# Kernel optimization log

Measured on AMD Instinct MI355X. Metric: run time of the kernel, lower is better.

Reference implementation:

```python
import jax, jax.numpy as jnp
import numpy as np

H = 4  # heads


def _tconv(x, src, dst, ea, Wq, bq, Wk, bk, Wv, bv, We, Ws, bs):
    # PyG TransformerConv, heads=4, concat=False, root_weight=True, beta=False
    N = x.shape[0]
    Dh = Wq.shape[1] // H  # per-head dim (= hidden_channels)
    q = (x @ Wq + bq).reshape(N, H, Dh)
    k = (x @ Wk + bk).reshape(N, H, Dh)
    v = (x @ Wv + bv).reshape(N, H, Dh)
    e = (ea @ We).reshape(-1, H, Dh)      # lin_edge has no bias in PyG
    kj = k[src] + e                        # [E, H, Dh]
    vj = v[src] + e                        # [E, H, Dh]
    alpha = (q[dst] * kj).sum(-1) / jnp.sqrt(jnp.asarray(Dh, x.dtype))  # [E, H]
    # segment softmax over incoming edges of each dst node
    m = jax.ops.segment_max(alpha, dst, num_segments=N)
    a = jnp.exp(alpha - m[dst])
    s = jax.ops.segment_sum(a, dst, num_segments=N)
    a = a / (s[dst] + 1e-16)
    out = jax.ops.segment_sum(a[:, :, None] * vj, dst, num_segments=N)  # [N, H, Dh]
    out = out.mean(axis=1)                 # concat=False -> mean over heads
    return out + x @ Ws + bs               # root/skip connection


def setup_inputs() -> dict:
    key = jax.random.key(0)
    ks = jax.random.split(key, 32)
    N, E, C_in, C_e, Ch = 50000, 800000, 32, 16, 32
    d = {}
    d['x'] = jax.random.normal(ks[0], (N, C_in), dtype=jnp.float32)
    d['edge_attr'] = jax.random.normal(ks[1], (E, C_e), dtype=jnp.float32)
    d['edge_index'] = jax.random.randint(ks[2], (2, E), 0, N, dtype=jnp.int32)
    s = 0.05
    i = 3
    for L, cin in ((1, C_in), (2, Ch)):
        d[f'Wq{L}'] = jax.random.normal(ks[i], (cin, H * Ch)) * s; i += 1
        d[f'bq{L}'] = jnp.zeros((H * Ch,), jnp.float32)
        d[f'Wk{L}'] = jax.random.normal(ks[i], (cin, H * Ch)) * s; i += 1
        d[f'bk{L}'] = jnp.zeros((H * Ch,), jnp.float32)
        d[f'Wv{L}'] = jax.random.normal(ks[i], (cin, H * Ch)) * s; i += 1
        d[f'bv{L}'] = jnp.zeros((H * Ch,), jnp.float32)
        d[f'We{L}'] = jax.random.normal(ks[i], (C_e, H * Ch)) * s; i += 1
        d[f'Ws{L}'] = jax.random.normal(ks[i], (cin, Ch)) * s; i += 1
        d[f'bs{L}'] = jnp.zeros((Ch,), jnp.float32)
    d['Wm1'] = jax.random.normal(ks[i], (2 * Ch + C_e, Ch)) * s; i += 1
    d['bm1'] = jnp.zeros((Ch,), jnp.float32)
    d['Wm2'] = jax.random.normal(ks[i], (Ch, 1)) * s; i += 1
    d['bm2'] = jnp.zeros((1,), jnp.float32)
    return d


def reference(x, edge_attr, edge_index,
              Wq1, bq1, Wk1, bk1, Wv1, bv1, We1, Ws1, bs1,
              Wq2, bq2, Wk2, bk2, Wv2, bv2, We2, Ws2, bs2,
              Wm1, bm1, Wm2, bm2):
    src, dst = edge_index[0], edge_index[1]
    h = jax.nn.relu(_tconv(x, src, dst, edge_attr, Wq1, bq1, Wk1, bk1, Wv1, bv1, We1, Ws1, bs1))
    h = jax.nn.relu(_tconv(h, src, dst, edge_attr, Wq2, bq2, Wk2, bk2, Wv2, bv2, We2, Ws2, bs2))
    ef = jnp.concatenate([h[src], edge_attr, h[dst]], axis=-1)  # [E, 2*Ch + C_e]
    out = jax.nn.relu(ef @ Wm1 + bm1) @ Wm2 + bm2
    return out.reshape(-1)
```

## Files before the change

kernel.cpp:

```cpp
#include <hip/hip_runtime.h>
#include <math.h>

#define D128 128
#define CH32 32
#define CE16 16

__global__ void k_hist(const int* __restrict__ dst, int* __restrict__ deg, int E) {
    int e = blockIdx.x * blockDim.x + threadIdx.x;
    if (e < E) atomicAdd(&deg[dst[e]], 1);
}

__global__ void k_scan1(const int* __restrict__ deg, int* __restrict__ offs,
                        int* __restrict__ bsum, int N) {
    __shared__ int buf[256];
    int t = threadIdx.x;
    int i = blockIdx.x * 256 + t;
    int v = (i < N) ? deg[i] : 0;
    buf[t] = v;
    __syncthreads();
    #pragma unroll
    for (int off = 1; off < 256; off <<= 1) {
        int val = (t >= off) ? buf[t - off] : 0;
        __syncthreads();
        buf[t] += val;
        __syncthreads();
    }
    if (i < N) offs[i] = buf[t] - v;
    if (t == 255) bsum[blockIdx.x] = buf[255];
}

__global__ void k_scan2(const int* __restrict__ bsum, int* __restrict__ boff, int nb) {
    __shared__ int buf[256];
    int t = threadIdx.x;
    int v = (t < nb) ? bsum[t] : 0;
    buf[t] = v;
    __syncthreads();
    #pragma unroll
    for (int off = 1; off < 256; off <<= 1) {
        int val = (t >= off) ? buf[t - off] : 0;
        __syncthreads();
        buf[t] += val;
        __syncthreads();
    }
    if (t < nb) boff[t] = buf[t] - v;
}

__global__ void k_scan3(const int* __restrict__ boff, int* __restrict__ offs,
                        int* __restrict__ cur, int N, int E) {
    int i = blockIdx.x * blockDim.x + threadIdx.x;
    if (i < N) {
        int o = offs[i] + boff[i >> 8];
        offs[i] = o;
        cur[i] = o;
    }
    if (i == 0) offs[N] = E;
}

__global__ void k_scatter(const int* __restrict__ src, const int* __restrict__ dst,
                          int* __restrict__ cur, int* __restrict__ csr_srcb,
                          float4* __restrict__ ea_csr4, const float4* __restrict__ ea4,
                          int E) {
    int e = blockIdx.x * blockDim.x + threadIdx.x;
    if (e < E) {
        int d = dst[e];
        int p = atomicAdd(&cur[d], 1);
        csr_srcb[p] = src[e] << 10;
        float4 a0 = ea4[e * 4 + 0];
        float4 a1 = ea4[e * 4 + 1];
        float4 a2 = ea4[e * 4 + 2];
        float4 a3 = ea4[e * 4 + 3];
        ea_csr4[p * 4 + 0] = a0;
        ea_csr4[p * 4 + 1] = a1;
        ea_csr4[p * 4 + 2] = a2;
        ea_csr4[p * 4 + 3] = a3;
    }
}

__global__ __launch_bounds__(128) void k_nodeproj(
    const float* __restrict__ xin,
    const float* __restrict__ Wq, const float* __restrict__ bq,
    const float* __restrict__ Wk, const float* __restrict__ bk,
    const float* __restrict__ Wv, const float* __restrict__ bv,
    const float* __restrict__ Ws, const float* __restrict__ bs,
    float* __restrict__ q, float* __restrict__ kv,
    float* __restrict__ skip, int N)
{
    int tid = threadIdx.x;
    int c   = tid & 31;
    float wq[32], wk[32], wv[32], ws[32];
    #pragma unroll
    for (int j = 0; j < 32; j++) {
        wq[j] = Wq[j * D128 + tid];
        wk[j] = Wk[j * D128 + tid];
        wv[j] = Wv[j * D128 + tid];
        ws[j] = Ws[j * CH32 + c];
    }
    float bqc = bq[tid], bkc = bk[tid], bvc = bv[tid], bsc = bs[c];
    __shared__ float xs[4][32];
    int nchunk = (N + 3) / 4;
    for (int chk = blockIdx.x; chk < nchunk; chk += gridDim.x) {
        int base = chk * 4;
        {
            int r = tid >> 5;
            int n = base + r;
            xs[r][c] = (n < N) ? xin[n * 32 + c] : 0.f;
        }
        __syncthreads();
        #pragma unroll
        for (int r = 0; r < 4; r++) {
            int n = base + r;
            if (n < N) {
                float aq = bqc, ak = bkc, av = bvc;
                #pragma unroll
                for (int j = 0; j < 32; j++) {
                    float xj = xs[r][j];
                    aq = fmaf(xj, wq[j], aq);
                    ak = fmaf(xj, wk[j], ak);
                    av = fmaf(xj, wv[j], av);
                }
                q[n * D128 + tid] = aq;
                kv[(size_t)n * 256 + tid]       = ak;
                kv[(size_t)n * 256 + 128 + tid] = av;
            }
        }
        {
            int r = tid >> 5;
            int n = base + r;
            if (n < N) {
                float as = bsc;
                #pragma unroll
                for (int j = 0; j < 32; j++) as = fmaf(xs[r][j], ws[j], as);
                skip[n * 32 + c] = as;
            }
        }
        __syncthreads();
    }
}

__global__ __launch_bounds__(64) void k_edgeattn(
    const float* __restrict__ q, const float* __restrict__ kv,
    const float* __restrict__ skip,
    const float* __restrict__ ea_csr, const float* __restrict__ We,
    const int* __restrict__ offs, const int* __restrict__ csr_srcb,
    float* __restrict__ hout)
{
    int node = blockIdx.x;
    int lane = threadIdx.x;
    int col2 = lane << 1;

    float2 we[16];
    #pragma unroll
    for (int j = 0; j < 16; j++)
        we[j] = *(const float2*)&We[j * D128 + col2];

    const float QS = 0.17677669529663687f * 1.4426950408889634f;
    float2 qv = *(const float2*)&q[(size_t)node * D128 + col2];
    qv.x *= QS; qv.y *= QS;

    int s0 = offs[node], s1 = offs[node + 1];

    float l = 0.f;
    float ac0 = 0.f, ac1 = 0.f;
    const char* kvb = (const char*)kv;
    int toff = lane * 8;

    int i = s0;
    if ((s1 - s0) & 1) {
        int sa = csr_srcb[i];
        const char* pa = kvb + (size_t)(unsigned)sa + toff;
        float2 ka = *(const float2*)(pa);
        float2 va = *(const float2*)(pa + 512);
        const float4* ea4 = (const float4*)&ea_csr[(size_t)i * 16];
        float4 a0 = ea4[0], a1 = ea4[1], a2 = ea4[2], a3 = ea4[3];

        float e0 = 0.f, e1 = 0.f;
        e0 = fmaf(a0.x, we[0].x,  e0);  e1 = fmaf(a0.x, we[0].y,  e1);
        e0 = fmaf(a0.y, we[1].x,  e0);  e1 = fmaf(a0.y, we[1].y,  e1);
        e0 = fmaf(a0.z, we[2].x,  e0);  e1 = fmaf(a0.z, we[2].y,  e1);
        e0 = fmaf(a0.w, we[3].x,  e0);  e1 = fmaf(a0.w, we[3].y,  e1);
        e0 = fmaf(a1.x, we[4].x,  e0);  e1 = fmaf(a1.x, we[4].y,  e1);
        e0 = fmaf(a1.y, we[5].x,  e0);  e1 = fmaf(a1.y, we[5].y,  e1);
        e0 = fmaf(a1.z, we[6].x,  e0);  e1 = fmaf(a1.z, we[6].y,  e1);
        e0 = fmaf(a1.w, we[7].x,  e0);  e1 = fmaf(a1.w, we[7].y,  e1);
        e0 = fmaf(a2.x, we[8].x,  e0);  e1 = fmaf(a2.x, we[8].y,  e1);
        e0 = fmaf(a2.y, we[9].x,  e0);  e1 = fmaf(a2.y, we[9].y,  e1);
        e0 = fmaf(a2.z, we[10].x, e0);  e1 = fmaf(a2.z, we[10].y, e1);
        e0 = fmaf(a2.w, we[11].x, e0);  e1 = fmaf(a2.w, we[11].y, e1);
        e0 = fmaf(a3.x, we[12].x, e0);  e1 = fmaf(a3.x, we[12].y, e1);
        e0 = fmaf(a3.y, we[13].x, e0);  e1 = fmaf(a3.y, we[13].y, e1);
        e0 = fmaf(a3.z, we[14].x, e0);  e1 = fmaf(a3.z, we[14].y, e1);
        e0 = fmaf(a3.w, we[15].x, e0);  e1 = fmaf(a3.w, we[15].y, e1);

        float kj0 = ka.x + e0, kj1 = ka.y + e1;
        float vj0 = va.x + e0, vj1 = va.y + e1;
        float t = qv.x * kj0;
        t = fmaf(qv.y, kj1, t);
        t += __shfl_xor(t, 1);
        t += __shfl_xor(t, 2);
        t += __shfl_xor(t, 4);
        t += __shfl_xor(t, 8);
        float p = __builtin_amdgcn_exp2f(t);
        l += p;
        ac0 = fmaf(p, vj0, ac0);
        ac1 = fmaf(p, vj1, ac1);
        i++;
    }

    for (; i < s1; i += 2) {
        int sa = csr_srcb[i];
        int sb = csr_srcb[i + 1];
        const char* pa = kvb + (size_t)(unsigned)sa + toff;
        const char* pb = kvb + (size_t)(unsigned)sb + toff;
        float2 ka = *(const float2*)(pa);
        float2 va = *(const float2*)(pa + 512);
        float2 kb = *(const float2*)(pb);
        float2 vb = *(const float2*)(pb + 512);
        const float4* ea4 = (const float4*)&ea_csr[(size_t)i * 16];
        float4 a0 = ea4[0], a1 = ea4[1], a2 = ea4[2], a3 = ea4[3];
        float4 b0 = ea4[4], b1 = ea4[5], b2 = ea4[6], b3 = ea4[7];

        float ea0 = 0.f, ea1 = 0.f, eb0 = 0.f, eb1 = 0.f;
        ea0 = fmaf(a0.x, we[0].x,  ea0);  ea1 = fmaf(a0.x, we[0].y,  ea1);
        eb0 = fmaf(b0.x, we[0].x,  eb0);  eb1 = fmaf(b0.x, we[0].y,  eb1);
        ea0 = fmaf(a0.y, we[1].x,  ea0);  ea1 = fmaf(a0.y, we[1].y,  ea1);
        eb0 = fmaf(b0.y, we[1].x,  eb0);  eb1 = fmaf(b0.y, we[1].y,  eb1);
        ea0 = fmaf(a0.z, we[2].x,  ea0);  ea1 = fmaf(a0.z, we[2].y,  ea1);
        eb0 = fmaf(b0.z, we[2].x,  eb0);  eb1 = fmaf(b0.z, we[2].y,  eb1);
        ea0 = fmaf(a0.w, we[3].x,  ea0);  ea1 = fmaf(a0.w, we[3].y,  ea1);
        eb0 = fmaf(b0.w, we[3].x,  eb0);  eb1 = fmaf(b0.w, we[3].y,  eb1);
        ea0 = fmaf(a1.x, we[4].x,  ea0);  ea1 = fmaf(a1.x, we[4].y,  ea1);
        eb0 = fmaf(b1.x, we[4].x,  eb0);  eb1 = fmaf(b1.x, we[4].y,  eb1);
        ea0 = fmaf(a1.y, we[5].x,  ea0);  ea1 = fmaf(a1.y, we[5].y,  ea1);
        eb0 = fmaf(b1.y, we[5].x,  eb0);  eb1 = fmaf(b1.y, we[5].y,  eb1);
        ea0 = fmaf(a1.z, we[6].x,  ea0);  ea1 = fmaf(a1.z, we[6].y,  ea1);
        eb0 = fmaf(b1.z, we[6].x,  eb0);  eb1 = fmaf(b1.z, we[6].y,  eb1);
        ea0 = fmaf(a1.w, we[7].x,  ea0);  ea1 = fmaf(a1.w, we[7].y,  ea1);
        eb0 = fmaf(b1.w, we[7].x,  eb0);  eb1 = fmaf(b1.w, we[7].y,  eb1);
        ea0 = fmaf(a2.x, we[8].x,  ea0);  ea1 = fmaf(a2.x, we[8].y,  ea1);
        eb0 = fmaf(b2.x, we[8].x,  eb0);  eb1 = fmaf(b2.x, we[8].y,  eb1);
        ea0 = fmaf(a2.y, we[9].x,  ea0);  ea1 = fmaf(a2.y, we[9].y,  ea1);
        eb0 = fmaf(b2.y, we[9].x,  eb0);  eb1 = fmaf(b2.y, we[9].y,  eb1);
        ea0 = fmaf(a2.z, we[10].x, ea0);  ea1 = fmaf(a2.z, we[10].y, ea1);
        eb0 = fmaf(b2.z, we[10].x, eb0);  eb1 = fmaf(b2.z, we[10].y, eb1);
        ea0 = fmaf(a2.w, we[11].x, ea0);  ea1 = fmaf(a2.w, we[11].y, ea1);
        eb0 = fmaf(b2.w, we[11].x, eb0);  eb1 = fmaf(b2.w, we[11].y, eb1);
        ea0 = fmaf(a3.x, we[12].x, ea0);  ea1 = fmaf(a3.x, we[12].y, ea1);
        eb0 = fmaf(b3.x, we[12].x, eb0);  eb1 = fmaf(b3.x, we[12].y, eb1);
        ea0 = fmaf(a3.y, we[13].x, ea0);  ea1 = fmaf(a3.y, we[13].y, ea1);
        eb0 = fmaf(b3.y, we[13].x, eb0);  eb1 = fmaf(b3.y, we[13].y, eb1);
        ea0 = fmaf(a3.z, we[14].x, ea0);  ea1 = fmaf(a3.z, we[14].y, ea1);
        eb0 = fmaf(b3.z, we[14].x, eb0);  eb1 = fmaf(b3.z, we[14].y, eb1);
        ea0 = fmaf(a3.w, we[15].x, ea0);  ea1 = fmaf(a3.w, we[15].y, ea1);
        eb0 = fmaf(b3.w, we[15].x, eb0);  eb1 = fmaf(b3.w, we[15].y, eb1);

        float kja0 = ka.x + ea0, kja1 = ka.y + ea1;
        float vja0 = va.x + ea0, vja1 = va.y + ea1;
        float kjb0 = kb.x + eb0, kjb1 = kb.y + eb1;
        float vjb0 = vb.x + eb0, vjb1 = vb.y + eb1;

        float ta = qv.x * kja0;
        float tb = qv.x * kjb0;
        ta = fmaf(qv.y, kja1, ta);
        tb = fmaf(qv.y, kjb1, tb);

        ta += __shfl_xor(ta, 1);   tb += __shfl_xor(tb, 1);
        ta += __shfl_xor(ta, 2);   tb += __shfl_xor(tb, 2);
        ta += __shfl_xor(ta, 4);   tb += __shfl_xor(tb, 4);
        ta += __shfl_xor(ta, 8);   tb += __shfl_xor(tb, 8);

        float p0 = __builtin_amdgcn_exp2f(ta);
        float p1 = __builtin_amdgcn_exp2f(tb);
        l += p0 + p1;
        ac0 = fmaf(p0, vja0, ac0);
        ac1 = fmaf(p0, vja1, ac1);
        ac0 = fmaf(p1, vjb0, ac0);
        ac1 = fmaf(p1, vjb1, ac1);
    }

    float inv = 1.0f / (l + 1e-16f);
    float r0 = ac0 * inv;
    float r1 = ac1 * inv;
    r0 += __shfl_xor(r0, 16);   r1 += __shfl_xor(r1, 16);
    r0 += __shfl_xor(r0, 32);   r1 += __shfl_xor(r1, 32);
    if (lane < 16) {
        const float2 sk = *(const float2*)&skip[(size_t)node * 32 + col2];
        float o0 = fmaxf(fmaf(0.25f, r0, sk.x), 0.f);
        float o1 = fmaxf(fmaf(0.25f, r1, sk.y), 0.f);
        *(float2*)&hout[(size_t)node * 32 + col2] = make_float2(o0, o1);
    }
}

__global__ __launch_bounds__(256) void k_mlp(
    const float* __restrict__ h, const float* __restrict__ ea,
    const int* __restrict__ src, const int* __restrict__ dst,
    const float* __restrict__ Wm1, const float* __restrict__ bm1,
    const float* __restrict__ Wm2, const float* __restrict__ bm2,
    float* __restrict__ out, int E)
{
    __shared__ float4 W4[80 * 8];
    __shared__ float bm1L[32];
    __shared__ float wm2L[32];
    int tid = threadIdx.x;
    const float4* Wm1_4 = (const float4*)Wm1;
    for (int i = tid; i < 640; i += 256) W4[i] = Wm1_4[i];
    if (tid < 32) { bm1L[tid] = bm1[tid]; wm2L[tid] = Wm2[tid]; }
    __syncthreads();

    int e = blockIdx.x * 256 + tid;
    if (e >= E) return;
    float b2 = bm2[0];
    int s = src[e], d = dst[e];

    float4 acc[8];
    #pragma unroll
    for (int i = 0; i < 8; i++) acc[i] = make_float4(0.f, 0.f, 0.f, 0.f);

    auto dorow = [&](int j, float xj) {
        #pragma unroll
        for (int c4 = 0; c4 < 8; c4++) {
            float4 w = W4[j * 8 + c4];
            acc[c4].x = fmaf(xj, w.x, acc[c4].x);
            acc[c4].y = fmaf(xj, w.y, acc[c4].y);
            acc[c4].z = fmaf(xj, w.z, acc[c4].z);
            acc[c4].w = fmaf(xj, w.w, acc[c4].w);
        }
    };

    const float4* hs  = (const float4*)(h + (size_t)s * 32);
    const float4* hd  = (const float4*)(h + (size_t)d * 32);
    const float4* eav = (const float4*)(ea + (size_t)e * 16);
    #pragma unroll
    for (int qd = 0; qd < 8; qd++) {
        float4 xv = hs[qd];
        dorow(qd * 4 + 0, xv.x); dorow(qd * 4 + 1, xv.y);
        dorow(qd * 4 + 2, xv.z); dorow(qd * 4 + 3, xv.w);
    }
    #pragma unroll
    for (int qd = 0; qd < 4; qd++) {
        float4 xv = eav[qd];
        dorow(32 + qd * 4 + 0, xv.x); dorow(32 + qd * 4 + 1, xv.y);
        dorow(32 + qd * 4 + 2, xv.z); dorow(32 + qd * 4 + 3, xv.w);
    }
    #pragma unroll
    for (int qd = 0; qd < 8; qd++) {
        float4 xv = hd[qd];
        dorow(48 + qd * 4 + 0, xv.x); dorow(48 + qd * 4 + 1, xv.y);
        dorow(48 + qd * 4 + 2, xv.z); dorow(48 + qd * 4 + 3, xv.w);
    }

    float y = b2;
    #pragma unroll
    for (int c4 = 0; c4 < 8; c4++) {
        y += fmaxf(acc[c4].x + bm1L[c4 * 4 + 0], 0.f) * wm2L[c4 * 4 + 0];
        y += fmaxf(acc[c4].y + bm1L[c4 * 4 + 1], 0.f) * wm2L[c4 * 4 + 1];
        y += fmaxf(acc[c4].z + bm1L[c4 * 4 + 2], 0.f) * wm2L[c4 * 4 + 2];
        y += fmaxf(acc[c4].w + bm1L[c4 * 4 + 3], 0.f) * wm2L[c4 * 4 + 3];
    }
    out[e] = y;
}

extern "C" void kernel_launch(void* const* d_in, const int* in_sizes, int n_in,
                              void* d_out, int out_size, void* d_ws, size_t ws_size,
                              hipStream_t stream)
{
    const float* x  = (const float*)d_in[0];
    const float* ea = (const float*)d_in[1];
    const int*   ei = (const int*)d_in[2];
    const int N = in_sizes[0] / 32;
    const int E = in_sizes[1] / 16;
    const int* src = ei;
    const int* dst = ei + E;

    const float *Wq1 = (const float*)d_in[3],  *bq1 = (const float*)d_in[4];
    const float *Wk1 = (const float*)d_in[5],  *bk1 = (const float*)d_in[6];
    const float *Wv1 = (const float*)d_in[7],  *bv1 = (const float*)d_in[8];
    const float *We1 = (const float*)d_in[9],  *Ws1 = (const float*)d_in[10];
    const float *bs1 = (const float*)d_in[11];
    const float *Wq2 = (const float*)d_in[12], *bq2 = (const float*)d_in[13];
    const float *Wk2 = (const float*)d_in[14], *bk2 = (const float*)d_in[15];
    const float *Wv2 = (const float*)d_in[16], *bv2 = (const float*)d_in[17];
    const float *We2 = (const float*)d_in[18], *Ws2 = (const float*)d_in[19];
    const float *bs2 = (const float*)d_in[20];
    const float *Wm1 = (const float*)d_in[21], *bm1 = (const float*)d_in[22];
    const float *Wm2 = (const float*)d_in[23], *bm2 = (const float*)d_in[24];

    char* w = (char*)d_ws;
    auto alloc = [&](size_t bytes) -> void* {
        void* p = (void*)w;
        w += (bytes + 255) & ~(size_t)255;
        return p;
    };
    int* deg      = (int*)alloc((size_t)N * 4);
    int* offs     = (int*)alloc(((size_t)N + 1) * 4);
    int* cur      = (int*)alloc((size_t)N * 4);
    int* bsum     = (int*)alloc(256 * 4);
    int* boff     = (int*)alloc(256 * 4);
    int* csr_srcb = (int*)alloc((size_t)E * 4);
    float* ea_csr = (float*)alloc((size_t)E * 16 * 4);
    float* qb     = (float*)alloc((size_t)N * 128 * 4);
    float* kvb    = (float*)alloc((size_t)N * 256 * 4);
    float* skipb  = (float*)alloc((size_t)N * 32 * 4);
    float* h1     = (float*)alloc((size_t)N * 32 * 4);
    float* h2     = (float*)alloc((size_t)N * 32 * 4);

    hipMemsetAsync(deg, 0, (size_t)N * 4, stream);

    int ebl = (E + 255) / 256;
    int nb  = (N + 255) / 256;
    k_hist<<<ebl, 256, 0, stream>>>(dst, deg, E);
    k_scan1<<<nb, 256, 0, stream>>>(deg, offs, bsum, N);
    k_scan2<<<1, 256, 0, stream>>>(bsum, boff, nb);
    k_scan3<<<nb, 256, 0, stream>>>(boff, offs, cur, N, E);
    k_scatter<<<ebl, 256, 0, stream>>>(src, dst, cur, csr_srcb,
                                       (float4*)ea_csr, (const float4*)ea, E);

    k_nodeproj<<<1024, 128, 0, stream>>>(x, Wq1, bq1, Wk1, bk1, Wv1, bv1, Ws1, bs1,
                                         qb, kvb, skipb, N);
    k_edgeattn<<<N, 64, 0, stream>>>(qb, kvb, skipb, ea_csr, We1,
                                     offs, csr_srcb, h1);
    k_nodeproj<<<1024, 128, 0, stream>>>(h1, Wq2, bq2, Wk2, bk2, Wv2, bv2, Ws2, bs2,
                                         qb, kvb, skipb, N);
    k_edgeattn<<<N, 64, 0, stream>>>(qb, kvb, skipb, ea_csr, We2,
                                     offs, csr_srcb, h2);
    k_mlp<<<ebl, 256, 0, stream>>>(h2, ea, src, dst, Wm1, bm1, Wm2, bm2,
                                   (float*)d_out, E);
}
```

Before: 607.4 us.

## Factor edge projection out of attention loop and interleave K/V layout

The edge-feature projection is moved out of the per-edge loop. q·(We·ea) is rewritten as (q·We)·ea using a per-head precomputed qe vector. The softmax-weighted sum of edge attributes is accumulated and multiplied by We once per node, which removes the 16×2 FMAs per edge. K and V are interleaved so each lane fetches both with a single float4 gather, and a two-deep software prefetch of source indices and features is added. This trades the unrolled two-edge loop for a serial single-edge loop with prefetch, which may reduce ILP.

```diff
diff --git a/kernel.cpp b/kernel.cpp
--- a/kernel.cpp
+++ b/kernel.cpp
@@ -87,6 +87,7 @@
 {
     int tid = threadIdx.x;
     int c   = tid & 31;
+    int pos = ((tid >> 1) << 2) | (tid & 1);
     float wq[32], wk[32], wv[32], ws[32];
     #pragma unroll
     for (int j = 0; j < 32; j++) {
@@ -119,8 +120,8 @@
                     av = fmaf(xj, wv[j], av);
                 }
                 q[n * D128 + tid] = aq;
-                kv[(size_t)n * 256 + tid]       = ak;
-                kv[(size_t)n * 256 + 128 + tid] = av;
+                kv[(size_t)n * 256 + pos]     = ak;
+                kv[(size_t)n * 256 + pos + 2] = av;
             }
         }
         {
@@ -147,6 +148,7 @@
     int node = blockIdx.x;
     int lane = threadIdx.x;
     int col2 = lane << 1;
+    int lan15 = lane & 15;
 
     float2 we[16];
     #pragma unroll
@@ -157,129 +159,71 @@
     float2 qv = *(const float2*)&q[(size_t)node * D128 + col2];
     qv.x *= QS; qv.y *= QS;
 
-    int s0 = offs[node], s1 = offs[node + 1];
-
-    float l = 0.f;
-    float ac0 = 0.f, ac1 = 0.f;
-    const char* kvb = (const char*)kv;
-    int toff = lane * 8;
-
-    int i = s0;
-    if ((s1 - s0) & 1) {
-        int sa = csr_srcb[i];
-        const char* pa = kvb + (size_t)(unsigned)sa + toff;
-        float2 ka = *(const float2*)(pa);
-        float2 va = *(const float2*)(pa + 512);
-        const float4* ea4 = (const float4*)&ea_csr[(size_t)i * 16];
-        float4 a0 = ea4[0], a1 = ea4[1], a2 = ea4[2], a3 = ea4[3];
-
-        float e0 = 0.f, e1 = 0.f;
-        e0 = fmaf(a0.x, we[0].x,  e0);  e1 = fmaf(a0.x, we[0].y,  e1);
-        e0 = fmaf(a0.y, we[1].x,  e0);  e1 = fmaf(a0.y, we[1].y,  e1);
-        e0 = fmaf(a0.z, we[2].x,  e0);  e1 = fmaf(a0.z, we[2].y,  e1);
-        e0 = fmaf(a0.w, we[3].x,  e0);  e1 = fmaf(a0.w, we[3].y,  e1);
-        e0 = fmaf(a1.x, we[4].x,  e0);  e1 = fmaf(a1.x, we[4].y,  e1);
-        e0 = fmaf(a1.y, we[5].x,  e0);  e1 = fmaf(a1.y, we[5].y,  e1);
-        e0 = fmaf(a1.z, we[6].x,  e0);  e1 = fmaf(a1.z, we[6].y,  e1);
-        e0 = fmaf(a1.w, we[7].x,  e0);  e1 = fmaf(a1.w, we[7].y,  e1);
-        e0 = fmaf(a2.x, we[8].x,  e0);  e1 = fmaf(a2.x, we[8].y,  e1);
-        e0 = fmaf(a2.y, we[9].x,  e0);  e1 = fmaf(a2.y, we[9].y,  e1);
-        e0 = fmaf(a2.z, we[10].x, e0);  e1 = fmaf(a2.z, we[10].y, e1);
-        e0 = fmaf(a2.w, we[11].x, e0);  e1 = fmaf(a2.w, we[11].y, e1);
-        e0 = fmaf(a3.x, we[12].x, e0);  e1 = fmaf(a3.x, we[12].y, e1);
-        e0 = fmaf(a3.y, we[13].x, e0);  e1 = fmaf(a3.y, we[13].y, e1);
-        e0 = fmaf(a3.z, we[14].x, e0);  e1 = fmaf(a3.z, we[14].y, e1);
-        e0 = fmaf(a3.w, we[15].x, e0);  e1 = fmaf(a3.w, we[15].y, e1);
-
-        float kj0 = ka.x + e0, kj1 = ka.y + e1;
-        float vj0 = va.x + e0, vj1 = va.y + e1;
-        float t = qv.x * kj0;
-        t = fmaf(qv.y, kj1, t);
+    float qe = 0.f;
+    #pragma unroll
+    for (int j = 0; j < 16; j++) {
+        float t = fmaf(qv.y, we[j].y, qv.x * we[j].x);
         t += __shfl_xor(t, 1);
         t += __shfl_xor(t, 2);
         t += __shfl_xor(t, 4);
         t += __shfl_xor(t, 8);
-        float p = __builtin_amdgcn_exp2f(t);
-        l += p;
-        ac0 = fmaf(p, vj0, ac0);
-        ac1 = fmaf(p, vj1, ac1);
-        i++;
-    }
-
-    for (; i < s1; i += 2) {
-        int sa = csr_srcb[i];
-        int sb = csr_srcb[i + 1];
-        const char* pa = kvb + (size_t)(unsigned)sa + toff;
-        const char* pb = kvb + (size_t)(unsigned)sb + toff;
-        float2 ka = *(const float2*)(pa);
-        float2 va = *(const float2*)(pa + 512);
-        float2 kb = *(const float2*)(pb);
-        float2 vb = *(const float2*)(pb + 512);
-        const float4* ea4 = (const float4*)&ea_csr[(size_t)i * 16];
-        float4 a0 = ea4[0], a1 = ea4[1], a2 = ea4[2], a3 = ea4[3];
-        float4 b0 = ea4[4], b1 = ea4[5], b2 = ea4[6], b3 = ea4[7];
-
-        float ea0 = 0.f, ea1 = 0.f, eb0 = 0.f, eb1 = 0.f;
-        ea0 = fmaf(a0.x, we[0].x,  ea0);  ea1 = fmaf(a0.x, we[0].y,  ea1);
-        eb0 = fmaf(b0.x, we[0].x,  eb0);  eb1 = fmaf(b0.x, we[0].y,  eb1);
-        ea0 = fmaf(a0.y, we[1].x,  ea0);  ea1 = fmaf(a0.y, we[1].y,  ea1);
-        eb0 = fmaf(b0.y, we[1].x,  eb0);  eb1 = fmaf(b0.y, we[1].y,  eb1);
-        ea0 = fmaf(a0.z, we[2].x,  ea0);  ea1 = fmaf(a0.z, we[2].y,  ea1);
-        eb0 = fmaf(b0.z, we[2].x,  eb0);  eb1 = fmaf(b0.z, we[2].y,  eb1);
-        ea0 = fmaf(a0.w, we[3].x,  ea0);  ea1 = fmaf(a0.w, we[3].y,  ea1);
-        eb0 = fmaf(b0.w, we[3].x,  eb0);  eb1 = fmaf(b0.w, we[3].y,  eb1);
-        ea0 = fmaf(a1.x, we[4].x,  ea0);  ea1 = fmaf(a1.x, we[4].y,  ea1);
-        eb0 = fmaf(b1.x, we[4].x,  eb0);  eb1 = fmaf(b1.x, we[4].y,  eb1);
-        ea0 = fmaf(a1.y, we[5].x,  ea0);  ea1 = fmaf(a1.y, we[5].y,  ea1);
-        eb0 = fmaf(b1.y, we[5].x,  eb0);  eb1 = fmaf(b1.y, we[5].y,  eb1);
-        ea0 = fmaf(a1.z, we[6].x,  ea0);  ea1 = fmaf(a1.z, we[6].y,  ea1);
-        eb0 = fmaf(b1.z, we[6].x,  eb0);  eb1 = fmaf(b1.z, we[6].y,  eb1);
-        ea0 = fmaf(a1.w, we[7].x,  ea0);  ea1 = fmaf(a1.w, we[7].y,  ea1);
-        eb0 = fmaf(b1.w, we[7].x,  eb0);  eb1 = fmaf(b1.w, we[7].y,  eb1);
-        ea0 = fmaf(a2.x, we[8].x,  ea0);  ea1 = fmaf(a2.x, we[8].y,  ea1);
-        eb0 = fmaf(b2.x, we[8].x,  eb0);  eb1 = fmaf(b2.x, we[8].y,  eb1);
-        ea0 = fmaf(a2.y, we[9].x,  ea0);  ea1 = fmaf(a2.y, we[9].y,  ea1);
-        eb0 = fmaf(b2.y, we[9].x,  eb0);  eb1 = fmaf(b2.y, we[9].y,  eb1);
-        ea0 = fmaf(a2.z, we[10].x, ea0);  ea1 = fmaf(a2.z, we[10].y, ea1);
-        eb0 = fmaf(b2.z, we[10].x, eb0);  eb1 = fmaf(b2.z, we[10].y, eb1);
-        ea0 = fmaf(a2.w, we[11].x, ea0);  ea1 = fmaf(a2.w, we[11].y, ea1);
-        eb0 = fmaf(b2.w, we[11].x, eb0);  eb1 = fmaf(b2.w, we[11].y, eb1);
-        ea0 = fmaf(a3.x, we[12].x, ea0);  ea1 = fmaf(a3.x, we[12].y, ea1);
-        eb0 = fmaf(b3.x, we[12].x, eb0);  eb1 = fmaf(b3.x, we[12].y, eb1);
-        ea0 = fmaf(a3.y, we[13].x, ea0);  ea1 = fmaf(a3.y, we[13].y, ea1);
-        eb0 = fmaf(b3.y, we[13].x, eb0);  eb1 = fmaf(b3.y, we[13].y, eb1);
-        ea0 = fmaf(a3.z, we[14].x, ea0);  ea1 = fmaf(a3.z, we[14].y, ea1);
-        eb0 = fmaf(b3.z, we[14].x, eb0);  eb1 = fmaf(b3.z, we[14].y, eb1);
-        ea0 = fmaf(a3.w, we[15].x, ea0);  ea1 = fmaf(a3.w, we[15].y, ea1);
-        eb0 = fmaf(b3.w, we[15].x, eb0);  eb1 = fmaf(b3.w, we[15].y, eb1);
-
-        float kja0 = ka.x + ea0, kja1 = ka.y + ea1;
-        float vja0 = va.x + ea0, vja1 = va.y + ea1;
-        float kjb0 = kb.x + eb0, kjb1 = kb.y + eb1;
-        float vjb0 = vb.x + eb0, vjb1 = vb.y + eb1;
-
-        float ta = qv.x * kja0;
-        float tb = qv.x * kjb0;
-        ta = fmaf(qv.y, kja1, ta);
-        tb = fmaf(qv.y, kjb1, tb);
-
-        ta += __shfl_xor(ta, 1);   tb += __shfl_xor(tb, 1);
-        ta += __shfl_xor(ta, 2);   tb += __shfl_xor(tb, 2);
-        ta += __shfl_xor(ta, 4);   tb += __shfl_xor(tb, 4);
-        ta += __shfl_xor(ta, 8);   tb += __shfl_xor(tb, 8);
-
-        float p0 = __builtin_amdgcn_exp2f(ta);
-        float p1 = __builtin_amdgcn_exp2f(tb);
-        l += p0 + p1;
-        ac0 = fmaf(p0, vja0, ac0);
-        ac1 = fmaf(p0, vja1, ac1);
-        ac0 = fmaf(p1, vjb0, ac0);
-        ac1 = fmaf(p1, vjb1, ac1);
+        if (lan15 == j) qe = t;
+    }
+
+    int s0 = offs[node], s1 = offs[node + 1];
+    int deg = s1 - s0;
+
+    float l = 0.f, ac0 = 0.f, ac1 = 0.f, sea = 0.f;
+
+    if (deg > 0) {
+        int last = s1 - 1;
+        const char* kvb = (const char*)kv;
+        int toff16 = lane << 4;
+
+        int j1 = min(s0 + 1, last);
+        int ib0 = csr_srcb[s0];
+        int ib1 = csr_srcb[j1];
+        float4 kv0 = *(const float4*)(kvb + (size_t)(unsigned)ib0 + toff16);
+        float4 kv1 = *(const float4*)(kvb + (size_t)(unsigned)ib1 + toff16);
+        float ea0 = ea_csr[(size_t)s0 * 16 + lan15];
+        float ea1 = ea_csr[(size_t)j1 * 16 + lan15];
+        int ib2 = csr_srcb[min(s0 + 2, last)];
+        int ib3 = csr_srcb[min(s0 + 3, last)];
+
+        for (int i = s0; i < s1; ++i) {
+            float4 kvN = *(const float4*)(kvb + (size_t)(unsigned)ib2 + toff16);
+            int in2 = min(i + 2, last);
+            float eaN = ea_csr[(size_t)in2 * 16 + lan15];
+            ib2 = ib3;
+            ib3 = csr_srcb[min(i + 4, last)];
+
+            float t = fmaf(qv.x, kv0.x, fmaf(qv.y, kv0.y, qe * ea0));
+            t += __shfl_xor(t, 1);
+            t += __shfl_xor(t, 2);
+            t += __shfl_xor(t, 4);
+            t += __shfl_xor(t, 8);
+            float p = __builtin_amdgcn_exp2f(t);
+            l += p;
+            ac0 = fmaf(p, kv0.z, ac0);
+            ac1 = fmaf(p, kv0.w, ac1);
+            sea = fmaf(p, ea0, sea);
+
+            kv0 = kv1; kv1 = kvN;
+            ea0 = ea1; ea1 = eaN;
+        }
     }
 
     float inv = 1.0f / (l + 1e-16f);
+    float se = sea * inv;
     float r0 = ac0 * inv;
     float r1 = ac1 * inv;
+    int gbase = lane & 48;
+    #pragma unroll
+    for (int j = 0; j < 16; j++) {
+        float sj = __shfl(se, gbase | j, 64);
+        r0 = fmaf(sj, we[j].x, r0);
+        r1 = fmaf(sj, we[j].y, r1);
+    }
     r0 += __shfl_xor(r0, 16);   r1 += __shfl_xor(r1, 16);
     r0 += __shfl_xor(r0, 32);   r1 += __shfl_xor(r1, 32);
     if (lane < 16) {
```

Result: no change. 618.9 us (+1.9%).
